# Performance work log

Measured on AMD Instinct MI355X. Metric: run time of the kernel, lower is better.

The kernel has to match this reference:

```python
import jax, jax.numpy as jnp
import numpy as np

_CLAMP = 1e6  # clamp bound for real/imag parts after each eml level
CPLX = jnp.complex64


def _eml_op(u, v):
    # eml(u, v) = exp(log(u) * log(v)) in complex arithmetic
    return jnp.exp(jnp.log(u) * jnp.log(v))


def _sanitize(z):
    r = jnp.clip(jnp.nan_to_num(z.real, nan=0.0, posinf=_CLAMP, neginf=-_CLAMP), -_CLAMP, _CLAMP)
    i = jnp.clip(jnp.nan_to_num(z.imag, nan=0.0, posinf=_CLAMP, neginf=-_CLAMP), -_CLAMP, _CLAMP)
    return jax.lax.complex(r, i)


def setup_inputs() -> dict:
    key = jax.random.key(0)
    k1, k2, k3 = jax.random.split(key, 3)
    depth = 10
    n_leaves = 2 ** depth          # 1024
    n_internal = n_leaves - 1      # 1023
    init_scale = 0.1
    batch = 65536
    x = jax.random.normal(k1, (batch,), jnp.float32)
    leaf = jax.random.normal(k2, (n_leaves, 2), jnp.float32) * init_scale
    leaf = leaf.at[:, 0].add(1.0)  # leaf_init[:, 0] += 1.0
    gate = jax.random.normal(k3, (n_internal, 2, 3), jnp.float32) * init_scale
    gate = gate.at[..., 2].add(1.0)  # gate_init[..., 2] += 1.0
    return {"x": x, "leaf_logits": leaf, "gate_logits": gate}


def reference(x, leaf_logits, gate_logits):
    xc = x.astype(CPLX)                      # [B]
    a = leaf_logits[:, 0].astype(CPLX)       # [L]
    b = leaf_logits[:, 1].astype(CPLX)       # [L]
    level = a[None, :] + b[None, :] * xc[:, None]   # [B, L] leaf inputs: alpha + beta*x
    x_b = xc[:, None]                        # [B, 1]
    g_all = gate_logits.astype(CPLX)         # [L-1, 2, 3]
    node_idx = 0
    while level.shape[1] > 1:
        n_pairs = level.shape[1] // 2
        left = level[:, 0::2]                # [B, n_pairs]
        right = level[:, 1::2]
        g = g_all[node_idx:node_idx + n_pairs]
        left_in = g[:, 0, 0][None] + g[:, 0, 1][None] * x_b + g[:, 0, 2][None] * left
        right_in = g[:, 1, 0][None] + g[:, 1, 1][None] * x_b + g[:, 1, 2][None] * right
        level = _sanitize(_eml_op(left_in, right_in))
        node_idx += n_pairs
    return level[:, 0]                       # [B] complex64
```

## Files before the change

### kernel.cpp

```cpp
#include <hip/hip_runtime.h>
#include <math.h>

#define CLAMPV 1000000.0f
#define PI_F     3.14159274f
#define HALFPI_F 1.57079633f
#define LN2_F    0.69314718f
#define L2E_F    1.44269504f
#define C1_F     0.17328680f
#define C2_F     0.05515890f
#define C2R_F    0.11031780f

typedef float v2f __attribute__((ext_vector_type(2)));

__device__ __forceinline__ v2f vb(float s) { return (v2f){s, s}; }
__device__ __forceinline__ v2f vfma(v2f a, v2f b, v2f c) { return __builtin_elementwise_fma(a, b, c); }

__device__ __forceinline__ const float* gptr(const float* __restrict__ g, int node) {
    return g + 6 * __builtin_amdgcn_readfirstlane(node);
}

__device__ __forceinline__ unsigned rank_below(unsigned long long m) {
    return __builtin_amdgcn_mbcnt_hi((unsigned)(m >> 32),
           __builtin_amdgcn_mbcnt_lo((unsigned)m, 0u));
}

__device__ __forceinline__ v2f fnode(v2f l, v2f r, v2f x,
                                     const float* __restrict__ g, v2f& tmin) {
    float g0 = g[0], g1 = g[1], g2 = g[2], g3 = g[3], g4 = g[4], g5 = g[5];
    v2f u = vfma(vb(g2), l, vfma(vb(g1), x, vb(g0)));
    v2f v = vfma(vb(g5), r, vfma(vb(g4), x, vb(g3)));
    tmin = __builtin_elementwise_min(tmin, __builtin_elementwise_min(u, v));
    v2f L2u = (v2f){__builtin_amdgcn_logf(u.x), __builtin_amdgcn_logf(u.y)};
    v2f L2v = (v2f){__builtin_amdgcn_logf(v.x), __builtin_amdgcn_logf(v.y)};
    v2f e = (vb(LN2_F) * L2u) * L2v;
    v2f rr = (v2f){__builtin_amdgcn_exp2f(e.x), __builtin_amdgcn_exp2f(e.y)};
    return __builtin_elementwise_min(rr, vb(CLAMPV));
}

__global__ __launch_bounds__(1024, 8) void eml_fast_taint(
    const float* __restrict__ x_g, const float* __restrict__ leaf_g,
    const float* __restrict__ gate_g, float* __restrict__ out,
    unsigned* __restrict__ cnt, unsigned* __restrict__ list,
    int batch, int out_real_only)
{
    __shared__ float4 s_t[16][64];

    const int lane = threadIdx.x;
    const int s    = threadIdx.y;
    const int e0 = blockIdx.x * 128 + lane;
    const v2f x2 = (v2f){x_g[e0], x_g[e0 + 64]};

    v2f tmin = vb(1.0f);
    v2f cA, cB, root;

#pragma clang loop unroll(disable)
    for (int q = 0; q < 4; ++q) {
        const int jq = 64 * s + 16 * q;
        v2f r2[2], h1, c;
#pragma unroll
        for (int p = 0; p < 4; ++p) {
            const int j = jq + 4 * p;
            const float* L = leaf_g + 2 * __builtin_amdgcn_readfirstlane(j);
            v2f l0 = vfma(vb(L[1]), x2, vb(L[0]));
            v2f l1 = vfma(vb(L[3]), x2, vb(L[2]));
            v2f l2 = vfma(vb(L[5]), x2, vb(L[4]));
            v2f l3 = vfma(vb(L[7]), x2, vb(L[6]));

            v2f A  = fnode(l0, l1, x2, gptr(gate_g, j >> 1), tmin);
            v2f B  = fnode(l2, l3, x2, gptr(gate_g, (j >> 1) + 1), tmin);
            v2f r1 = fnode(A, B, x2, gptr(gate_g, 512 + (j >> 2)), tmin);
            if (p & 1) r2[p >> 1] = fnode(h1, r1, x2, gptr(gate_g, 768 + (j >> 3)), tmin);
            else       h1 = r1;
        }
        c = fnode(r2[0], r2[1], x2, gptr(gate_g, 896 + (jq >> 4)), tmin);
        if      (q == 0) cA = c;
        else if (q == 1) cB = fnode(cA, c, x2, gptr(gate_g, 960 + 2 * s), tmin);
        else if (q == 2) cA = c;
        else {
            v2f t = fnode(cA, c, x2, gptr(gate_g, 961 + 2 * s), tmin);
            root  = fnode(cB, t, x2, gptr(gate_g, 992 + s), tmin);
        }
    }

    s_t[s][lane] = make_float4(root.x, root.y, tmin.x, tmin.y);
    __syncthreads();
    if (s != 0) return;

#pragma clang loop unroll(disable)
    for (int L = 6; L <= 9; ++L) {
        const int cntL = 1 << (9 - L);
        const int base = 1024 - (1 << (10 - L));
#pragma clang loop unroll(disable)
        for (int j = 0; j < cntL; ++j) {
            float4 a = s_t[2 * j][lane], b = s_t[2 * j + 1][lane];
            v2f tm = __builtin_elementwise_min((v2f){a.z, a.w}, (v2f){b.z, b.w});
            v2f r  = fnode((v2f){a.x, a.y}, (v2f){b.x, b.y}, x2,
                           gptr(gate_g, base + j), tm);
            s_t[j][lane] = make_float4(r.x, r.y, tm.x, tm.y);
        }
    }

    float4 fin = s_t[0][lane];
    const bool t0 = !(fin.z > 0.0f);
    const bool t1 = !(fin.w > 0.0f);

    if (!t0) {
        if (out_real_only) out[e0] = fin.x;
        else reinterpret_cast<float2*>(out)[e0] = make_float2(fin.x, 0.0f);
    }
    if (!t1) {
        if (out_real_only) out[e0 + 64] = fin.y;
        else reinterpret_cast<float2*>(out)[e0 + 64] = make_float2(fin.y, 0.0f);
    }

    unsigned long long m0 = __ballot(t0), m1 = __ballot(t1);
    int n0 = __popcll(m0), n1 = __popcll(m1);
    unsigned base = 0;
    if (lane == 0 && (n0 + n1)) base = atomicAdd(cnt, (unsigned)(n0 + n1));
    base = __shfl(base, 0);
    if (t0) list[base + rank_below(m0)] = (unsigned)e0;
    if (t1) list[base + n0 + rank_below(m1)] = (unsigned)(e0 + 64);
}


__device__ __forceinline__ v2f sanitv(v2f v) {
    v2f c;
    c.x = __builtin_amdgcn_fmed3f(v.x, -CLAMPV, CLAMPV);
    c.y = __builtin_amdgcn_fmed3f(v.y, -CLAMPV, CLAMPV);
    c.x = (v.x != v.x) ? 0.0f : c.x;
    c.y = (v.y != v.y) ? 0.0f : c.y;
    return c;
}

__device__ __forceinline__ v2f fatan2v(v2f y, v2f x) {
    v2f ax = __builtin_elementwise_abs(x);
    v2f ay = __builtin_elementwise_abs(y);
    v2f mx = __builtin_elementwise_max(ax, ay);
    v2f mn = __builtin_elementwise_min(ax, ay);
    v2f r  = (v2f){__builtin_amdgcn_rcpf(mx.x), __builtin_amdgcn_rcpf(mx.y)};
    v2f t  = mn * r;
    v2f z  = t * t;
    v2f p  = vfma(z, vfma(z, vfma(z, vfma(z,
             vb(0.02083510f), vb(-0.08513300f)), vb(0.18014100f)), vb(-0.33029950f)),
             vb(0.99986600f));
    p = p * t;
    p.x = (ay.x > ax.x) ? (HALFPI_F - p.x) : p.x;
    p.y = (ay.y > ax.y) ? (HALFPI_F - p.y) : p.y;
    p.x = (x.x < 0.0f) ? (PI_F - p.x) : p.x;
    p.y = (x.y < 0.0f) ? (PI_F - p.y) : p.y;
    p.x = copysignf(p.x, y.x);
    p.y = copysignf(p.y, y.y);
    return p;
}

__device__ __forceinline__ void exp_tailv(v2f e, v2f f0, v2f& ore, v2f& oim) {
    v2f r = (v2f){__builtin_amdgcn_exp2f(e.x), __builtin_amdgcn_exp2f(e.y)};
    v2f f = (v2f){__builtin_amdgcn_fractf(f0.x), __builtin_amdgcn_fractf(f0.y)};
    v2f sn = (v2f){__builtin_amdgcn_sinf(f.x), __builtin_amdgcn_sinf(f.y)};
    v2f cs = (v2f){__builtin_amdgcn_cosf(f.x), __builtin_amdgcn_cosf(f.y)};
    ore = sanitv(r * cs);
    oim = sanitv(r * sn);
}

__device__ __forceinline__ void fast_rp(v2f ure, v2f vre, v2f& ore, v2f& oim) {
    v2f L2u = (v2f){__builtin_amdgcn_logf(ure.x), __builtin_amdgcn_logf(ure.y)};
    v2f L2v = (v2f){__builtin_amdgcn_logf(vre.x), __builtin_amdgcn_logf(vre.y)};
    v2f e = (vb(LN2_F) * L2u) * L2v;
    v2f r = (v2f){__builtin_amdgcn_exp2f(e.x), __builtin_amdgcn_exp2f(e.y)};
    v2f c = __builtin_elementwise_min(r, vb(CLAMPV));
    c.x = (r.x != r.x) ? 0.0f : c.x;
    c.y = (r.y != r.y) ? 0.0f : c.y;
    ore = c;
    oim = vb(0.0f);
}

__device__ __forceinline__ void node_any(
    v2f lre, v2f lim, v2f rre, v2f rim,
    v2f x, const float* __restrict__ g,
    v2f& ore, v2f& oim)
{
    float g0 = g[0], g1 = g[1], g2 = g[2], g3 = g[3], g4 = g[4], g5 = g[5];
    v2f ure = vfma(vb(g2), lre, vfma(vb(g1), x, vb(g0)));
    v2f vre = vfma(vb(g5), rre, vfma(vb(g4), x, vb(g3)));
    v2f mn = __builtin_elementwise_min(ure, vre);

    unsigned long long bad =
        __ballot(lim.x != 0.0f) | __ballot(lim.y != 0.0f) |
        __ballot(rim.x != 0.0f) | __ballot(rim.y != 0.0f) |
        __ballot(mn.x <= 0.0f)  | __ballot(mn.y <= 0.0f);

    if (bad == 0ULL) {
        fast_rp(ure, vre, ore, oim);
    } else {
        v2f uim = vfma(vb(g2), lim, vb(0.0f));
        v2f vim = vfma(vb(g5), rim, vb(0.0f));

        v2f nu = vfma(ure, ure, uim * uim);
        v2f nv = vfma(vre, vre, vim * vim);
        v2f L2u = (v2f){__builtin_amdgcn_logf(nu.x), __builtin_amdgcn_logf(nu.y)};
        v2f L2v = (v2f){__builtin_amdgcn_logf(nv.x), __builtin_amdgcn_logf(nv.y)};
        v2f Au = fatan2v(uim, ure);
        v2f Av = fatan2v(vim, vre);

        v2f t2 = vb(L2E_F) * (Au * Av);
        v2f e  = vfma(vb(C1_F) * L2u, L2v, -t2);
        v2f s2 = vfma(L2u, Av, Au * L2v);
        v2f f0 = vb(C2_F) * s2;
        exp_tailv(e, f0, ore, oim);
    }
}

__device__ __forceinline__ void node_r0(
    v2f l, v2f r, v2f x, const float* __restrict__ g,
    v2f& ore, v2f& oim)
{
    float g0 = g[0], g1 = g[1], g2 = g[2], g3 = g[3], g4 = g[4], g5 = g[5];
    v2f u = vfma(vb(g2), l, vfma(vb(g1), x, vb(g0)));
    v2f v = vfma(vb(g5), r, vfma(vb(g4), x, vb(g3)));
    v2f mn = __builtin_elementwise_min(u, v);

    unsigned long long bad = __ballot(mn.x <= 0.0f) | __ballot(mn.y <= 0.0f);

    if (bad == 0ULL) {
        fast_rp(u, v, ore, oim);
    } else {
        v2f au = __builtin_elementwise_abs(u);
        v2f av = __builtin_elementwise_abs(v);
        v2f L2u = (v2f){__builtin_amdgcn_logf(au.x), __builtin_amdgcn_logf(au.y)};
        v2f L2v = (v2f){__builtin_amdgcn_logf(av.x), __builtin_amdgcn_logf(av.y)};
        v2f Au, Av;
        Au.x = (u.x < 0.0f) ? PI_F : 0.0f;
        Au.y = (u.y < 0.0f) ? PI_F : 0.0f;
        Av.x = (v.x < 0.0f) ? PI_F : 0.0f;
        Av.y = (v.y < 0.0f) ? PI_F : 0.0f;

        v2f t2 = vb(L2E_F) * (Au * Av);
        v2f e  = vfma(vb(LN2_F) * L2u, L2v, -t2);
        v2f s2 = vfma(L2u, Av, Au * L2v);
        v2f f0 = vb(C2R_F) * s2;
        exp_tailv(e, f0, ore, oim);
    }
}

__global__ __launch_bounds__(1024, 8) void eml_slow(
    const float* __restrict__ x_g, const float* __restrict__ leaf_g,
    const float* __restrict__ gate_g, const unsigned* __restrict__ cnt,
    const unsigned* __restrict__ list, float* __restrict__ out,
    int batch, int out_real_only)
{
    __shared__ float4 s_t[16][64];

    const unsigned count = cnt[0];
    const unsigned r0 = blockIdx.x * 128u;
    if (r0 >= count) return;

    const int lane = threadIdx.x;
    const int s    = threadIdx.y;
    const unsigned ra = min(r0 + (unsigned)lane, count - 1u);
    const unsigned rb = min(r0 + (unsigned)lane + 64u, count - 1u);
    const unsigned ia = list[ra], ib = list[rb];
    const v2f x2 = (v2f){x_g[ia], x_g[ib]};

    v2f cAre, cAim, cBre, cBim, rootre, rootim;

#pragma clang loop unroll(disable)
    for (int q = 0; q < 4; ++q) {
        const int jq = 64 * s + 16 * q;
        v2f r2re[2], r2im[2];
        v2f h1re = vb(0.0f), h1im = vb(0.0f);
        v2f cre, cim;

#pragma unroll
        for (int p = 0; p < 4; ++p) {
            const int j = jq + 4 * p;
            const float* L = leaf_g + 2 * __builtin_amdgcn_readfirstlane(j);
            v2f l0 = vfma(vb(L[1]), x2, vb(L[0]));
            v2f l1 = vfma(vb(L[3]), x2, vb(L[2]));
            v2f l2 = vfma(vb(L[5]), x2, vb(L[4]));
            v2f l3 = vfma(vb(L[7]), x2, vb(L[6]));

            v2f Are, Aim, Bre, Bim;
            node_r0(l0, l1, x2, gptr(gate_g, j >> 1), Are, Aim);
            node_r0(l2, l3, x2, gptr(gate_g, (j >> 1) + 1), Bre, Bim);

            v2f r1re, r1im;
            node_any(Are, Aim, Bre, Bim, x2, gptr(gate_g, 512 + (j >> 2)), r1re, r1im);

            if (p & 1) {
                node_any(h1re, h1im, r1re, r1im, x2,
                         gptr(gate_g, 768 + (j >> 3)), r2re[p >> 1], r2im[p >> 1]);
            } else {
                h1re = r1re; h1im = r1im;
            }
        }
        v2f cre2, cim2;
        node_any(r2re[0], r2im[0], r2re[1], r2im[1], x2,
                 gptr(gate_g, 896 + (jq >> 4)), cre2, cim2);
        cre = cre2; cim = cim2;

        if (q == 0) {
            cAre = cre; cAim = cim;
        } else if (q == 1) {
            node_any(cAre, cAim, cre, cim, x2, gptr(gate_g, 960 + 2 * s), cBre, cBim);
        } else if (q == 2) {
            cAre = cre; cAim = cim;
        } else {
            v2f tre, tim;
            node_any(cAre, cAim, cre, cim, x2, gptr(gate_g, 961 + 2 * s), tre, tim);
            node_any(cBre, cBim, tre, tim, x2, gptr(gate_g, 992 + s), rootre, rootim);
        }
    }

    s_t[s][lane] = make_float4(rootre.x, rootre.y, rootim.x, rootim.y);
    __syncthreads();
    if (s != 0) return;

#pragma clang loop unroll(disable)
    for (int L = 6; L <= 9; ++L) {
        const int cntL = 1 << (9 - L);
        const int base = 1024 - (1 << (10 - L));
#pragma clang loop unroll(disable)
        for (int j = 0; j < cntL; ++j) {
            float4 a = s_t[2 * j][lane], b = s_t[2 * j + 1][lane];
            v2f rre, rim;
            node_any((v2f){a.x, a.y}, (v2f){a.z, a.w},
                     (v2f){b.x, b.y}, (v2f){b.z, b.w},
                     x2, gptr(gate_g, base + j), rre, rim);
            s_t[j][lane] = make_float4(rre.x, rre.y, rim.x, rim.y);
        }
    }

    float4 fin = s_t[0][lane];
    if (out_real_only) {
        out[ia] = fin.x;
        out[ib] = fin.y;
    } else {
        reinterpret_cast<float2*>(out)[ia] = make_float2(fin.x, fin.z);
        reinterpret_cast<float2*>(out)[ib] = make_float2(fin.y, fin.w);
    }
}

extern "C" void kernel_launch(void* const* d_in, const int* in_sizes, int n_in,
                              void* d_out, int out_size, void* d_ws, size_t ws_size,
                              hipStream_t stream) {
    const float* x    = (const float*)d_in[0];
    const float* leaf = (const float*)d_in[1];
    const float* gate = (const float*)d_in[2];
    float* out = (float*)d_out;
    const int batch = in_sizes[0];

    const int out_real_only = (out_size == batch) ? 1 : 0;

    unsigned* cnt  = (unsigned*)d_ws;
    unsigned* list = (unsigned*)d_ws + 64;

    hipMemsetAsync(cnt, 0, sizeof(unsigned), stream);

    dim3 block(64, 16);
    dim3 grid(batch / 128);
    hipLaunchKernelGGL(eml_fast_taint, grid, block, 0, stream,
                       x, leaf, gate, out, cnt, list, batch, out_real_only);
    hipLaunchKernelGGL(eml_slow, grid, block, 0, stream,
                       x, leaf, gate, cnt, list, out, batch, out_real_only);
}
```

Measured before the change: 128.8 us.

## Bucket-sort tainted slow-path elements by x to improve wavefront coherence

Adds a single-block counting-sort kernel that orders the list of elements needing the slow complex path by the high bits of their x value before the slow kernel processes them. Neighbouring lanes then handle similar x values, which is meant to reduce branch divergence and uneven work within each wavefront in the slow path. The cost is an extra launch, and the sort runs in one workgroup with shared-memory atomics, so it is serialized and may add latency if the list is long. The sort only runs when the workspace is large enough to hold a second list.

```diff
diff --git a/kernel.cpp b/kernel.cpp
--- a/kernel.cpp
+++ b/kernel.cpp
@@ -17,6 +17,12 @@
 
 __device__ __forceinline__ const float* gptr(const float* __restrict__ g, int node) {
     return g + 6 * __builtin_amdgcn_readfirstlane(node);
+}
+
+__device__ __forceinline__ unsigned sortkey(float x) {
+    unsigned u = __float_as_uint(x);
+    u ^= (unsigned)(((int)u) >> 31) | 0x80000000u;
+    return u;
 }
 
 __device__ __forceinline__ unsigned rank_below(unsigned long long m) {
@@ -120,6 +126,45 @@
     base = __shfl(base, 0);
     if (t0) list[base + rank_below(m0)] = (unsigned)e0;
     if (t1) list[base + n0 + rank_below(m1)] = (unsigned)(e0 + 64);
+}
+
+__global__ __launch_bounds__(1024) void eml_sort(
+    const float* __restrict__ x_g, const unsigned* __restrict__ cnt,
+    const unsigned* __restrict__ list, unsigned* __restrict__ list2)
+{
+    __shared__ unsigned hist[4096];
+    __shared__ unsigned part[1024];
+    const unsigned n = cnt[0];
+    const int t = threadIdx.x;
+
+    for (int i = t; i < 4096; i += 1024) hist[i] = 0u;
+    __syncthreads();
+    for (unsigned i = t; i < n; i += 1024)
+        atomicAdd(&hist[sortkey(x_g[list[i]]) >> 20], 1u);
+    __syncthreads();
+
+    unsigned h0 = hist[4*t], h1 = hist[4*t+1], h2 = hist[4*t+2], h3 = hist[4*t+3];
+    unsigned sum = h0 + h1 + h2 + h3;
+    part[t] = sum;
+    __syncthreads();
+    for (int d = 1; d < 1024; d <<= 1) {
+        unsigned v = (t >= d) ? part[t - d] : 0u;
+        __syncthreads();
+        part[t] += v;
+        __syncthreads();
+    }
+    unsigned excl = part[t] - sum;
+    hist[4*t]   = excl;
+    hist[4*t+1] = excl + h0;
+    hist[4*t+2] = excl + h0 + h1;
+    hist[4*t+3] = excl + h0 + h1 + h2;
+    __syncthreads();
+
+    for (unsigned i = t; i < n; i += 1024) {
+        unsigned id = list[i];
+        unsigned pos = atomicAdd(&hist[sortkey(x_g[id]) >> 20], 1u);
+        list2[pos] = id;
+    }
 }
 
 
@@ -293,10 +338,8 @@
                 h1re = r1re; h1im = r1im;
             }
         }
-        v2f cre2, cim2;
         node_any(r2re[0], r2im[0], r2re[1], r2im[1], x2,
-                 gptr(gate_g, 896 + (jq >> 4)), cre2, cim2);
-        cre = cre2; cim = cim2;
+                 gptr(gate_g, 896 + (jq >> 4)), cre, cim);
 
         if (q == 0) {
             cAre = cre; cAim = cim;
@@ -351,8 +394,11 @@
 
     const int out_real_only = (out_size == batch) ? 1 : 0;
 
-    unsigned* cnt  = (unsigned*)d_ws;
-    unsigned* list = (unsigned*)d_ws + 64;
+    unsigned* cnt   = (unsigned*)d_ws;
+    unsigned* list  = (unsigned*)d_ws + 64;
+    unsigned* list2 = list + batch;
+    const size_t need_sort = (64 + 2 * (size_t)batch) * sizeof(unsigned);
+    const bool do_sort = (ws_size >= need_sort);
 
     hipMemsetAsync(cnt, 0, sizeof(unsigned), stream);
 
@@ -360,6 +406,11 @@
     dim3 grid(batch / 128);
     hipLaunchKernelGGL(eml_fast_taint, grid, block, 0, stream,
                        x, leaf, gate, out, cnt, list, batch, out_real_only);
+    if (do_sort) {
+        hipLaunchKernelGGL(eml_sort, dim3(1), dim3(1024), 0, stream,
+                           x, cnt, list, list2);
+    }
     hipLaunchKernelGGL(eml_slow, grid, block, 0, stream,
-                       x, leaf, gate, cnt, list, out, batch, out_real_only);
-}
+                       x, leaf, gate, cnt,
+                       do_sort ? list2 : list, out, batch, out_real_only);
+}
```

Result: slower. 136.1 us (+5.6%).
